# Kernel tuning notes

Measured on AMD Instinct MI355X. Metric: run time of the kernel, lower is better.

Reference implementation:

```python
import jax, jax.numpy as jnp
import numpy as np

N_NODES = 1_000_000
N_EDGES = 16_000_000
N_GRAPHS = 10_000
NUM_FEAT = 8
HIDDEN = 64
OUT_DIM = 1
EMB_ROWS = 5
EMB_DIM = NUM_FEAT - 3  # 5


def setup_inputs() -> dict:
    key = jax.random.key(0)
    ks = jax.random.split(key, 10)
    pos = jax.random.normal(ks[0], (N_NODES, 3), dtype=jnp.float32)
    z = jax.random.randint(ks[1], (N_NODES,), 0, EMB_ROWS)
    edge_index = jax.random.randint(ks[2], (2, N_EDGES), 0, N_NODES)
    batch = jnp.sort(jax.random.randint(ks[3], (N_NODES,), 0, N_GRAPHS))
    # learned parameters
    emb = jax.random.normal(ks[4], (EMB_ROWS, EMB_DIM), dtype=jnp.float32)
    s1 = 1.0 / np.sqrt(NUM_FEAT)
    W1 = jax.random.uniform(ks[5], (NUM_FEAT, HIDDEN), minval=-s1, maxval=s1, dtype=jnp.float32)
    b1 = jnp.zeros((HIDDEN,), dtype=jnp.float32)
    s2 = 1.0 / np.sqrt(HIDDEN)
    W2 = jax.random.uniform(ks[6], (HIDDEN, HIDDEN), minval=-s2, maxval=s2, dtype=jnp.float32)
    b2 = jnp.zeros((HIDDEN,), dtype=jnp.float32)
    fcW = jax.random.uniform(ks[7], (HIDDEN, OUT_DIM), minval=-s2, maxval=s2, dtype=jnp.float32)
    fcb = jnp.zeros((OUT_DIM,), dtype=jnp.float32)
    return {"pos": pos, "z": z, "edge_index": edge_index, "batch": batch,
            "emb": emb, "W1": W1, "b1": b1, "W2": W2, "b2": b2,
            "fcW": fcW, "fcb": fcb}


def reference(pos, z, edge_index, batch, emb, W1, b1, W2, b2, fcW, fcb):
    # node features: [pos | embedding(z)] -> [N, 8]
    x = jnp.concatenate([pos, emb[z]], axis=-1)
    # GINConv (eps=0): h_i = MLP(x_i + sum_{j->i} x_j)
    src, dst = edge_index[0], edge_index[1]
    agg = jax.ops.segment_sum(x[src], dst, num_segments=N_NODES)  # [N, 8]
    h = x + agg
    h = jax.nn.relu(h @ W1 + b1)
    h = h @ W2 + b2
    h = jax.nn.relu(h)
    # global add pool over graphs
    pooled = jax.ops.segment_sum(h, batch, num_segments=N_GRAPHS)  # [G, 64]
    return pooled @ fcW + fcb  # [G, 1]
```

## Files before the change

### kernel.cpp

```cpp
#include <hip/hip_runtime.h>
#include <stdint.h>


#define N_NODES  1000000
#define N_EDGES  16000000
#define N_GRAPHS 10000
#define NB       1024
#define NBUCK    977
#define BCAP     18432
#define EPB      16384
#define PBLK     977
#define PSCALE   65536.0f
#define PINV     (1.0f / 65536.0f)

__global__ __launch_bounds__(256) void k_features(
    const float* __restrict__ pos, const int* __restrict__ z,
    uint2* __restrict__ px2)
{
    int i = blockIdx.x * 256 + threadIdx.x;
    if (i >= N_NODES) return;
    float x = pos[i * 3 + 0], y = pos[i * 3 + 1], w = pos[i * 3 + 2];
    x = fminf(fmaxf(x, -7.99f), 7.99f);
    y = fminf(fmaxf(y, -7.99f), 7.99f);
    w = fminf(fmaxf(w, -7.99f), 7.99f);
    uint32_t ux = (uint32_t)__float2int_rn(x * PSCALE) & 0xFFFFFu;
    uint32_t uy = (uint32_t)__float2int_rn(y * PSCALE) & 0xFFFFFu;
    uint32_t uz = (uint32_t)__float2int_rn(w * PSCALE) & 0xFFFFFu;
    uint32_t zi = (uint32_t)z[i];
    uint2 r;
    r.x = ux | (uy << 20);
    r.y = (uy >> 12) | (uz << 8) | (zi << 28);
    px2[i] = r;
}

__global__ __launch_bounds__(256) void k_init(
    const float* __restrict__ fcb, float* __restrict__ out, int* __restrict__ cursor)
{
    int i = blockIdx.x * 256 + threadIdx.x;
    if (i < N_GRAPHS) out[i] = fcb[0];
    if (i < NB) cursor[i] = 0;
}

__global__ __launch_bounds__(512) void k_partition(
    const int* __restrict__ ei, int* __restrict__ cursor, uint32_t* __restrict__ perm)
{
    __shared__ uint32_t sVal[EPB];
    __shared__ int sHist[NB];
    __shared__ int sGB[NB];
    __shared__ int sCur[NB];
    __shared__ int sScan[512];

    int t = threadIdx.x;
    int e0 = blockIdx.x * EPB;
    int nE = N_EDGES - e0; if (nE > EPB) nE = EPB;

    for (int c = t; c < NB; c += 512) sHist[c] = 0;
    __syncthreads();

    const int4* src4 = (const int4*)ei;
    const int4* dst4 = (const int4*)(ei + N_EDGES);
    int i40 = e0 >> 2;

    #pragma unroll
    for (int jj = 0; jj < EPB / 2048; jj++) {
        int i4 = i40 + jj * 512 + t;
        if (i4 * 4 < N_EDGES) {
            int4 d = dst4[i4];
            atomicAdd(&sHist[d.x >> 10], 1);
            atomicAdd(&sHist[d.y >> 10], 1);
            atomicAdd(&sHist[d.z >> 10], 1);
            atomicAdd(&sHist[d.w >> 10], 1);
        }
    }
    __syncthreads();

    #pragma unroll
    for (int k = 0; k < 2; k++) {
        int c = t * 2 + k;
        int cnt = sHist[c];
        sGB[c] = cnt ? atomicAdd(&cursor[c], cnt) : 0;
    }
    int pt = sHist[t * 2] + sHist[t * 2 + 1];
    sScan[t] = pt;
    __syncthreads();
    for (int off = 1; off < 512; off <<= 1) {
        int v = (t >= off) ? sScan[t - off] : 0;
        __syncthreads();
        sScan[t] += v;
        __syncthreads();
    }
    int base = (t == 0) ? 0 : sScan[t - 1];
    #pragma unroll
    for (int k = 0; k < 2; k++) {
        int c = t * 2 + k;
        int cnt = sHist[c];
        sHist[c] = base;
        sCur[c]  = base;
        base += cnt;
    }
    __syncthreads();

    #pragma unroll
    for (int jj = 0; jj < EPB / 2048; jj++) {
        int i4 = i40 + jj * 512 + t;
        if (i4 * 4 < N_EDGES) {
            int4 s = src4[i4];
            int4 d = dst4[i4];
            int b, p;
            b = d.x >> 10; p = atomicAdd(&sCur[b], 1);
            sVal[p] = ((uint32_t)s.x << 10) | (uint32_t)(d.x & 1023);
            b = d.y >> 10; p = atomicAdd(&sCur[b], 1);
            sVal[p] = ((uint32_t)s.y << 10) | (uint32_t)(d.y & 1023);
            b = d.z >> 10; p = atomicAdd(&sCur[b], 1);
            sVal[p] = ((uint32_t)s.z << 10) | (uint32_t)(d.z & 1023);
            b = d.w >> 10; p = atomicAdd(&sCur[b], 1);
            sVal[p] = ((uint32_t)s.w << 10) | (uint32_t)(d.w & 1023);
        }
    }
    __syncthreads();

    for (int j = t; j < nE; j += 512) {
        uint32_t v = sVal[j];
        int lo = 0;
        #pragma unroll
        for (int st = 512; st; st >>= 1) {
            int cand = lo + st;
            if (cand < NB && sHist[cand] <= j) lo = cand;
        }
        int off = j - sHist[lo];
        perm[(size_t)lo * BCAP + sGB[lo] + off] = v;
    }
}

__device__ __forceinline__ float mlp_node(
    const float* __restrict__ sW1T, const float* __restrict__ b1,
    const float4* __restrict__ W2v, const float* __restrict__ b2,
    const float* __restrict__ fcW, const float f[8])
{
    const float4* w1t = (const float4*)sW1T;
    float s = 0.0f;
    #pragma unroll
    for (int oc = 0; oc < 4; oc++) {
        float a[16];
        #pragma unroll
        for (int i2 = 0; i2 < 16; i2++) a[i2] = b2[oc * 16 + i2];
        for (int k = 0; k < 64; k++) {
            float4 wa = w1t[k * 2 + 0];
            float4 wb = w1t[k * 2 + 1];
            float h = b1[k];
            h = fmaf(f[0], wa.x, h); h = fmaf(f[1], wa.y, h);
            h = fmaf(f[2], wa.z, h); h = fmaf(f[3], wa.w, h);
            h = fmaf(f[4], wb.x, h); h = fmaf(f[5], wb.y, h);
            h = fmaf(f[6], wb.z, h); h = fmaf(f[7], wb.w, h);
            h = fmaxf(h, 0.0f);
            #pragma unroll
            for (int v4 = 0; v4 < 4; v4++) {
                float4 w = W2v[k * 16 + oc * 4 + v4];
                a[v4*4+0] = fmaf(h, w.x, a[v4*4+0]);
                a[v4*4+1] = fmaf(h, w.y, a[v4*4+1]);
                a[v4*4+2] = fmaf(h, w.z, a[v4*4+2]);
                a[v4*4+3] = fmaf(h, w.w, a[v4*4+3]);
            }
        }
        #pragma unroll
        for (int i2 = 0; i2 < 16; i2++)
            s += fmaxf(a[i2], 0.0f) * fcW[oc * 16 + i2];
    }
    return s;
}

__device__ __forceinline__ int dec_x(uint2 g) {
    return ((int)(g.x << 12)) >> 12;
}
__device__ __forceinline__ int dec_y(uint2 g) {
    uint32_t uy = (g.x >> 20) | ((g.y & 0xFFu) << 12);
    return ((int)(uy << 12)) >> 12;
}
__device__ __forceinline__ int dec_z(uint2 g) {
    return ((int)(((g.y >> 8) & 0xFFFFFu) << 12)) >> 12;
}

__global__ __launch_bounds__(512) void k_bucket_mlp(
    const uint32_t* __restrict__ perm, const int* __restrict__ cursor,
    const uint2* __restrict__ px2, const float* __restrict__ emb,
    const int* __restrict__ batch,
    const float* __restrict__ W1, const float* __restrict__ b1,
    const float* __restrict__ W2, const float* __restrict__ b2,
    const float* __restrict__ fcW, float* __restrict__ out)
{
    __shared__ int sAcc[1024 * 5];
    __shared__ float sW1T[512];
    __shared__ float sEmb[25];

    int t = threadIdx.x;
    int b = blockIdx.x;

    for (int j = t; j < 1024 * 5; j += 512) sAcc[j] = 0;
    {
        int j = t >> 6, k = t & 63;
        sW1T[k * 8 + j] = W1[j * 64 + k];
    }
    if (t < 25) sEmb[t] = emb[t];
    __syncthreads();

    int n = cursor[b];
    if (n > BCAP) n = BCAP;
    const uint32_t* pb = perm + (size_t)b * BCAP;

    #pragma unroll 4
    for (int j = t; j < n; j += 512) {
        uint32_t p = pb[j];
        uint2 g = px2[p >> 10];
        int* s = sAcc + (p & 1023u) * 5;
        atomicAdd(s + 0, dec_x(g));
        atomicAdd(s + 1, dec_y(g));
        atomicAdd(s + 2, dec_z(g));
        atomicAdd((unsigned int*)(s + 3), 1u << (6 * (g.y >> 28)));
    }
    __syncthreads();

    const float4* W2v = (const float4*)W2;
    float* redS = (float*)sAcc;
    int*   redG = sAcc + 1024;

    float s0 = 0.0f; int g0 = -1;
    {
        int q = t;
        int node = (b << 10) + q;
        if (node < N_NODES) {
            uint2 me = px2[node];
            int mz = (int)(me.y >> 28);
            const int* sa = sAcc + q * 5;
            unsigned int pk = (unsigned int)sa[3];
            float f[8];
            f[0] = (float)(dec_x(me) + sa[0]) * PINV;
            f[1] = (float)(dec_y(me) + sa[1]) * PINV;
            f[2] = (float)(dec_z(me) + sa[2]) * PINV;
            float c0 = (float)(pk & 63u);
            float c1 = (float)((pk >> 6) & 63u);
            float c2 = (float)((pk >> 12) & 63u);
            float c3 = (float)((pk >> 18) & 63u);
            float c4 = (float)((pk >> 24) & 63u);
            #pragma unroll
            for (int e = 0; e < 5; e++) {
                f[3 + e] = sEmb[mz * 5 + e]
                         + c0 * sEmb[e]      + c1 * sEmb[5 + e]
                         + c2 * sEmb[10 + e] + c3 * sEmb[15 + e]
                         + c4 * sEmb[20 + e];
            }
            s0 = mlp_node(sW1T, b1, W2v, b2, fcW, f);
            g0 = batch[node];
        }
    }
    __syncthreads();
    redS[t] = s0; redG[t] = g0;

    float s1 = 0.0f; int g1 = -1;
    {
        int q = t + 512;
        int node = (b << 10) + q;
        if (node < N_NODES) {
            uint2 me = px2[node];
            int mz = (int)(me.y >> 28);
            const int* sa = sAcc + q * 5;
            unsigned int pk = (unsigned int)sa[3];
            float f[8];
            f[0] = (float)(dec_x(me) + sa[0]) * PINV;
            f[1] = (float)(dec_y(me) + sa[1]) * PINV;
            f[2] = (float)(dec_z(me) + sa[2]) * PINV;
            float c0 = (float)(pk & 63u);
            float c1 = (float)((pk >> 6) & 63u);
            float c2 = (float)((pk >> 12) & 63u);
            float c3 = (float)((pk >> 18) & 63u);
            float c4 = (float)((pk >> 24) & 63u);
            #pragma unroll
            for (int e = 0; e < 5; e++) {
                f[3 + e] = sEmb[mz * 5 + e]
                         + c0 * sEmb[e]      + c1 * sEmb[5 + e]
                         + c2 * sEmb[10 + e] + c3 * sEmb[15 + e]
                         + c4 * sEmb[20 + e];
            }
            s1 = mlp_node(sW1T, b1, W2v, b2, fcW, f);
            g1 = batch[node];
        }
    }
    __syncthreads();
    redS[t + 512] = s1; redG[t + 512] = g1;
    __syncthreads();

    #pragma unroll
    for (int w = 0; w < 2; w++) {
        int idx = t + w * 512;
        int g = redG[idx];
        if (g >= 0 && (idx == 0 || redG[idx - 1] != g)) {
            float sum = redS[idx];
            for (int j = idx + 1; j < 1024 && redG[j] == g; j++) sum += redS[j];
            unsafeAtomicAdd(&out[g], sum);
        }
    }
}

extern "C" void kernel_launch(void* const* d_in, const int* in_sizes, int n_in,
                              void* d_out, int out_size, void* d_ws, size_t ws_size,
                              hipStream_t stream) {
    const float* pos  = (const float*)d_in[0];
    const int*   z    = (const int*)  d_in[1];
    const int*   ei   = (const int*)  d_in[2];
    const int*   batch= (const int*)  d_in[3];
    const float* emb  = (const float*)d_in[4];
    const float* W1   = (const float*)d_in[5];
    const float* b1   = (const float*)d_in[6];
    const float* W2   = (const float*)d_in[7];
    const float* b2   = (const float*)d_in[8];
    const float* fcW  = (const float*)d_in[9];
    const float* fcb  = (const float*)d_in[10];
    float* out = (float*)d_out;

    uint2*    px2    = (uint2*)d_ws;
    uint32_t* perm   = (uint32_t*)((char*)d_ws + (size_t)N_NODES * 8);
    int*      cursor = (int*)(perm + (size_t)NB * BCAP);

    k_features <<<(N_NODES + 255) / 256, 256, 0, stream>>>(pos, z, px2);
    k_init     <<<(N_GRAPHS + 255) / 256, 256, 0, stream>>>(fcb, out, cursor);
    k_partition<<<PBLK, 512, 0, stream>>>(ei, cursor, perm);
    k_bucket_mlp<<<NBUCK, 512, 0, stream>>>(perm, cursor, px2, emb, batch,
                                            W1, b1, W2, b2, fcW, out);
}
```

Before: 597.7 us.

## Split destination buckets by source half and vectorize gather reads

Within each destination bucket, edges are partitioned by whether the source node falls in the lower or upper half of the node range. Lower-half edges are stored from the front of the bucket and upper-half edges from the back, tracked by two packed 16-bit global cursors. The gather kernel then walks each half with uint4 loads, so the px2 reads for nearby threads are drawn from a narrower source range, aiming for better cache locality. This adds packed counter arithmetic and more branching in the partition kernel, and it depends on per-block counts fitting in 16 bits.

```diff
diff --git a/kernel.cpp b/kernel.cpp
--- a/kernel.cpp
+++ b/kernel.cpp
@@ -12,6 +12,7 @@
 #define PBLK     977
 #define PSCALE   65536.0f
 #define PINV     (1.0f / 65536.0f)
+#define SRCMID   500000
 
 __global__ __launch_bounds__(256) void k_features(
     const float* __restrict__ pos, const int* __restrict__ z,
@@ -38,7 +39,7 @@
 {
     int i = blockIdx.x * 256 + threadIdx.x;
     if (i < N_GRAPHS) out[i] = fcb[0];
-    if (i < NB) cursor[i] = 0;
+    if (i < 2 * NB) cursor[i] = 0;
 }
 
 __global__ __launch_bounds__(512) void k_partition(
@@ -50,6 +51,9 @@
     __shared__ int sCur[NB];
     __shared__ int sScan[512];
 
+    int* cursorA = cursor;
+    int* cursorB = cursor + NB;
+
     int t = threadIdx.x;
     int e0 = blockIdx.x * EPB;
     int nE = N_EDGES - e0; if (nE > EPB) nE = EPB;
@@ -65,22 +69,27 @@
     for (int jj = 0; jj < EPB / 2048; jj++) {
         int i4 = i40 + jj * 512 + t;
         if (i4 * 4 < N_EDGES) {
+            int4 s = src4[i4];
             int4 d = dst4[i4];
-            atomicAdd(&sHist[d.x >> 10], 1);
-            atomicAdd(&sHist[d.y >> 10], 1);
-            atomicAdd(&sHist[d.z >> 10], 1);
-            atomicAdd(&sHist[d.w >> 10], 1);
-        }
-    }
-    __syncthreads();
-
+            atomicAdd(&sHist[d.x >> 10], (s.x < SRCMID) ? 1 : 65536);
+            atomicAdd(&sHist[d.y >> 10], (s.y < SRCMID) ? 1 : 65536);
+            atomicAdd(&sHist[d.z >> 10], (s.z < SRCMID) ? 1 : 65536);
+            atomicAdd(&sHist[d.w >> 10], (s.w < SRCMID) ? 1 : 65536);
+        }
+    }
+    __syncthreads();
+
+    int pt = 0;
     #pragma unroll
     for (int k = 0; k < 2; k++) {
         int c = t * 2 + k;
-        int cnt = sHist[c];
-        sGB[c] = cnt ? atomicAdd(&cursor[c], cnt) : 0;
-    }
-    int pt = sHist[t * 2] + sHist[t * 2 + 1];
+        uint32_t h = (uint32_t)sHist[c];
+        int c0 = (int)(h & 0xFFFFu), c1 = (int)(h >> 16);
+        int gb0 = c0 ? atomicAdd(&cursorA[c], c0) : 0;
+        int gb1 = c1 ? atomicAdd(&cursorB[c], c1) : 0;
+        sGB[c] = gb0 | (gb1 << 16);
+        pt += c0 + c1;
+    }
     sScan[t] = pt;
     __syncthreads();
     for (int off = 1; off < 512; off <<= 1) {
@@ -93,9 +102,10 @@
     #pragma unroll
     for (int k = 0; k < 2; k++) {
         int c = t * 2 + k;
-        int cnt = sHist[c];
+        uint32_t h = (uint32_t)sHist[c];
+        int cnt = (int)(h & 0xFFFFu) + (int)(h >> 16);
         sHist[c] = base;
-        sCur[c]  = base;
+        sCur[c]  = base | ((base + cnt - 1) << 16);
         base += cnt;
     }
     __syncthreads();
@@ -106,15 +116,22 @@
         if (i4 * 4 < N_EDGES) {
             int4 s = src4[i4];
             int4 d = dst4[i4];
-            int b, p;
-            b = d.x >> 10; p = atomicAdd(&sCur[b], 1);
-            sVal[p] = ((uint32_t)s.x << 10) | (uint32_t)(d.x & 1023);
-            b = d.y >> 10; p = atomicAdd(&sCur[b], 1);
-            sVal[p] = ((uint32_t)s.y << 10) | (uint32_t)(d.y & 1023);
-            b = d.z >> 10; p = atomicAdd(&sCur[b], 1);
-            sVal[p] = ((uint32_t)s.z << 10) | (uint32_t)(d.z & 1023);
-            b = d.w >> 10; p = atomicAdd(&sCur[b], 1);
-            sVal[p] = ((uint32_t)s.w << 10) | (uint32_t)(d.w & 1023);
+            int b; uint32_t old, p;
+            #define SCAT(SS, DD)                                              \
+                b = (DD) >> 10;                                               \
+                if ((SS) < SRCMID) {                                          \
+                    old = (uint32_t)atomicAdd(&sCur[b], 1);                   \
+                    p = old & 0xFFFFu;                                        \
+                } else {                                                      \
+                    old = (uint32_t)atomicAdd(&sCur[b], -65536);              \
+                    p = old >> 16;                                            \
+                }                                                             \
+                sVal[p] = ((uint32_t)(SS) << 10) | (uint32_t)((DD) & 1023);
+            SCAT(s.x, d.x)
+            SCAT(s.y, d.y)
+            SCAT(s.z, d.z)
+            SCAT(s.w, d.w)
+            #undef SCAT
         }
     }
     __syncthreads();
@@ -127,8 +144,20 @@
             int cand = lo + st;
             if (cand < NB && sHist[cand] <= j) lo = cand;
         }
-        int off = j - sHist[lo];
-        perm[(size_t)lo * BCAP + sGB[lo] + off] = v;
+        int lstart = sHist[lo];
+        int off = j - lstart;
+        int n0l = (int)((uint32_t)sCur[lo] & 0xFFFFu) - lstart;
+        uint32_t gb = (uint32_t)sGB[lo];
+        size_t dest;
+        if (off < n0l) {
+            dest = (size_t)lo * BCAP + (gb & 0xFFFFu) + off;
+        } else {
+            int cnt = ((lo < NB - 1) ? sHist[lo + 1] : nE) - lstart;
+            int n1l = cnt - n0l;
+            int gb1 = (int)(gb >> 16);
+            dest = (size_t)lo * BCAP + (BCAP - gb1 - n1l) + (off - n0l);
+        }
+        perm[dest] = v;
     }
 }
 
@@ -203,20 +232,41 @@
     if (t < 25) sEmb[t] = emb[t];
     __syncthreads();
 
-    int n = cursor[b];
-    if (n > BCAP) n = BCAP;
+    int n0 = cursor[b];
+    int n1 = cursor[NB + b];
+    if (n0 > BCAP) n0 = BCAP;
+    if (n1 > BCAP - n0) n1 = BCAP - n0;
     const uint32_t* pb = perm + (size_t)b * BCAP;
-
-    #pragma unroll 4
-    for (int j = t; j < n; j += 512) {
-        uint32_t p = pb[j];
-        uint2 g = px2[p >> 10];
-        int* s = sAcc + (p & 1023u) * 5;
-        atomicAdd(s + 0, dec_x(g));
-        atomicAdd(s + 1, dec_y(g));
-        atomicAdd(s + 2, dec_z(g));
-        atomicAdd((unsigned int*)(s + 3), 1u << (6 * (g.y >> 28)));
-    }
+    const uint4* pb4 = (const uint4*)pb;
+
+    #define GPROC(P)                                                          \
+        {   uint32_t p_ = (P);                                                \
+            uint2 g_ = px2[p_ >> 10];                                         \
+            int* s_ = sAcc + (p_ & 1023u) * 5;                                \
+            atomicAdd(s_ + 0, dec_x(g_));                                     \
+            atomicAdd(s_ + 1, dec_y(g_));                                     \
+            atomicAdd(s_ + 2, dec_z(g_));                                     \
+            atomicAdd((unsigned int*)(s_ + 3), 1u << (6 * (g_.y >> 28)));     \
+        }
+    {
+        int n04 = n0 >> 2;
+        #pragma unroll 2
+        for (int j = t; j < n04; j += 512) {
+            uint4 q = pb4[j];
+            GPROC(q.x) GPROC(q.y) GPROC(q.z) GPROC(q.w)
+        }
+        for (int j = (n04 << 2) + t; j < n0; j += 512) GPROC(pb[j])
+        int n14 = n1 >> 2;
+        int q0 = (BCAP >> 2) - n14;
+        #pragma unroll 2
+        for (int j = t; j < n14; j += 512) {
+            uint4 q = pb4[q0 + j];
+            GPROC(q.x) GPROC(q.y) GPROC(q.z) GPROC(q.w)
+        }
+        int head = n1 & 3;
+        for (int j = t; j < head; j += 512) GPROC(pb[BCAP - n1 + j])
+    }
+    #undef GPROC
     __syncthreads();
 
     const float4* W2v = (const float4*)W2;
```

After: 587.5 us. About the same (-1.7%).
